# Optimization experiments

Hardware: AMD Instinct MI355X
Metric: run time of the kernel (lower is better)

## Reference

```python
import jax, jax.numpy as jnp
import numpy as np
from jax import lax

HEADS = 8
DIM_HEAD = 64
MODALITIES = 8
QUERY_DIM = 128
INNER = HEADS * DIM_HEAD  # 512


def _conv(x, w):
    # x: (b, Cin, H, W), w: (Cout, Cin, kh, kw), VALID padding (padding done manually)
    return lax.conv_general_dilated(x, w, window_strides=(1, 1), padding='VALID',
                                    dimension_numbers=('NCHW', 'OIHW', 'NCHW'))


def _reflect_pad_w(x):
    # ReflectionPad2d((2,2,0,0)): pad width (last) axis by 2 on each side
    return jnp.pad(x, ((0, 0), (0, 0), (0, 0), (2, 2)), mode='reflect')


def setup_inputs() -> dict:
    key = jax.random.key(0)
    k1, k2, k3, k4 = jax.random.split(key, 4)
    b, n, m, c = 2, 4096, MODALITIES, QUERY_DIM
    x = jax.random.normal(k1, (b, n, m, c), dtype=jnp.float32)
    Wq = jax.random.normal(k2, (INNER, c, 1, 5), dtype=jnp.float32) * 0.02
    Wkv = jax.random.normal(k3, (2 * INNER, c, 1, 5), dtype=jnp.float32) * 0.02
    Wout = jax.random.normal(k4, (c * m, INNER, m, 5), dtype=jnp.float32) * 0.02
    return {"x": x, "Wq": Wq, "Wkv": Wkv, "Wout": Wout}


def reference(x, Wq, Wkv, Wout):
    b, n, m, c = x.shape
    h, d = HEADS, DIM_HEAD
    scale = d ** -0.5

    xp = _reflect_pad_w(jnp.transpose(x, (0, 3, 2, 1)))  # (b, c, m, n+4)
    q = _conv(xp, Wq)                                     # (b, h*d, m, n)
    kv = _conv(xp, Wkv)                                   # (b, 2*h*d, m, n)
    k, v = kv[:, :h * d], kv[:, h * d:]

    # channel axis (h d) split: h outer, d inner -> (b, h, d, m, n)
    q = q.reshape(b, h, d, m, n)
    k = k.reshape(b, h, d, m, n)
    v = v.reshape(b, h, d, m, n)

    # attention over sequence axis n; feature dim is (m d) per head
    sim = jnp.einsum('bhdmi,bhdmj->bhij', q, k) * scale   # (b, h, n, n)
    attn = jax.nn.softmax(sim, axis=-1)
    out = jnp.einsum('bhij,bhdmj->bhdmi', attn, v)        # (b, h, d, m, n)

    out = out.reshape(b, h * d, m, n)                     # 'b (h d) m n'
    o = _conv(_reflect_pad_w(out), Wout)                  # (b, c*m, 1, n)
    o = o.reshape(b, c, m, 1, n)[:, :, :, 0, :]           # squeeze height-1 dim -> (b, c, m, n)
    return o.reshape(x.shape)                             # torch .view(x_shape) is a raw reshape
```

## Files before the change

kernel.cpp:

```cpp
#include <hip/hip_runtime.h>
#include <stdint.h>


typedef __attribute__((ext_vector_type(8))) short short8;
typedef __attribute__((ext_vector_type(4))) short short4v;
typedef __attribute__((ext_vector_type(2))) short short2v;
typedef __attribute__((ext_vector_type(4))) float f32x4;
typedef __attribute__((ext_vector_type(16))) float f32x16;

__device__ __forceinline__ f32x4 mfma16(short8 a, short8 b, f32x4 c) {
  return __builtin_amdgcn_mfma_f32_16x16x32_bf16(a, b, c, 0, 0, 0);
}
__device__ __forceinline__ f32x16 mfma32(short8 a, short8 b, f32x16 c) {
  return __builtin_amdgcn_mfma_f32_32x32x16_bf16(a, b, c, 0, 0, 0);
}

__device__ __forceinline__ unsigned short f2bf(float f) {
  union { float f; uint32_t u; } v; v.f = f;
  uint32_t r = (v.u + 0x7fffu + ((v.u >> 16) & 1u)) >> 16;
  return (unsigned short)r;
}

__device__ __forceinline__ uint32_t cvtpk(float lo, float hi) {
  uint32_t r;
  asm volatile("v_cvt_pk_bf16_f32 %0, %1, %2" : "=v"(r) : "v"(lo), "v"(hi));
  return r;
}
__device__ __forceinline__ void plswap(uint32_t& a, uint32_t& b) {
  asm volatile("v_permlane32_swap_b32 %0, %1" : "+v"(a), "+v"(b));
}

__device__ __forceinline__ int refl4096(int p) {
  p = p < 0 ? -p : p;
  return p >= 4096 ? 8190 - p : p;
}

__device__ __forceinline__ void gl_lds16(const void* g, void* l) {
  __builtin_amdgcn_global_load_lds(
      (const __attribute__((address_space(1))) void*)g,
      (__attribute__((address_space(3))) void*)l, 16, 0, 0);
}

__global__ void k_convw_qkv(const float* __restrict__ Wq,
                            const float* __restrict__ Wkv,
                            unsigned short* __restrict__ out) {
  int e = blockIdx.x * 256 + threadIdx.x;
  int oc = e / 640, k = e - oc * 640;
  int ci = k & 127, t = k >> 7;
  float w = (oc < 512) ? Wq[oc * 640 + ci * 5 + t]
                       : Wkv[(oc - 512) * 640 + ci * 5 + t];
  out[e] = f2bf(w);
}

__global__ __launch_bounds__(256)
void k_convx(const float* __restrict__ x, unsigned short* __restrict__ xb,
             int b) {
  int e = (blockIdx.x * 256 + threadIdx.x) * 8;
  const float* src = x + (size_t)b * 4194304 + e;
  f32x4 v0 = *(const f32x4*)src;
  f32x4 v1 = *(const f32x4*)(src + 4);
  short8 pk;
  pk[0] = (short)f2bf(v0[0]); pk[1] = (short)f2bf(v0[1]);
  pk[2] = (short)f2bf(v0[2]); pk[3] = (short)f2bf(v0[3]);
  pk[4] = (short)f2bf(v1[0]); pk[5] = (short)f2bf(v1[1]);
  pk[6] = (short)f2bf(v1[2]); pk[7] = (short)f2bf(v1[3]);
  *(short8*)(xb + e) = pk;
}

__global__ __launch_bounds__(256)
void k_convw_out(const float* __restrict__ Wout,
                 unsigned short* __restrict__ out) {
  __shared__ unsigned short row_l[20480];
  const int oc = blockIdx.x;
  const int tid = threadIdx.x;
  const float* src = Wout + (size_t)oc * 20480;
#pragma unroll
  for (int i0 = 0; i0 < 5120; i0 += 256) {
    int i = i0 + tid;
    f32x4 v = *(const f32x4*)(src + (size_t)i * 4);
    short4v pk;
    pk[0] = (short)f2bf(v[0]); pk[1] = (short)f2bf(v[1]);
    pk[2] = (short)f2bf(v[2]); pk[3] = (short)f2bf(v[3]);
    *(short4v*)(row_l + i * 4) = pk;
  }
  __syncthreads();
  unsigned short* drow = out + (size_t)oc * 20480;
#pragma unroll
  for (int r0 = 0; r0 < 20480; r0 += 512) {
    int e = r0 + tid * 2;
    int t0 = e >> 12, ft0 = e & 4095;
    int t1 = (e + 1) >> 12, ft1 = (e + 1) & 4095;
    short2v pk;
    pk[0] = (short)row_l[(ft0 >> 3) * 40 + (ft0 & 7) * 5 + t0];
    pk[1] = (short)row_l[(ft1 >> 3) * 40 + (ft1 & 7) * 5 + t1];
    *(short2v*)(drow + e) = pk;
  }
}

__global__ __launch_bounds__(256, 2)
void k_qkv(const unsigned short* __restrict__ xb,
           const unsigned short* __restrict__ Wb,
           unsigned short* __restrict__ Qg, unsigned short* __restrict__ Kg,
           unsigned short* __restrict__ Vg) {
  __shared__ __align__(16) unsigned short As[128 * 64];
  __shared__ __align__(16) unsigned short Bs[128 * 64];
  const int tid = threadIdx.x;
  const int lane = tid & 63, w = tid >> 6;
  const int wr = w >> 1, wc = w & 1;
  const int l15 = lane & 15, lg = lane >> 4;
  const int p0 = blockIdx.x * 128;
  const int ocb = blockIdx.y * 128;
  const int m = blockIdx.z;

  f32x4 acc[4][4];
#pragma unroll
  for (int i = 0; i < 4; i++)
#pragma unroll
    for (int j = 0; j < 4; j++) acc[i][j] = (f32x4){0.f, 0.f, 0.f, 0.f};

  for (int ks = 0; ks < 10; ks++) {
    const int t = ks >> 1;
    const int ci0 = (ks & 1) << 6;
    __syncthreads();
#pragma unroll
    for (int i = 0; i < 4; i++) {
      int s = tid + (i << 8);
      int row = s >> 3, c = s & 7;
      int cs = c ^ (row & 7);
      int xn = refl4096(p0 + row - 2 + t);
      gl_lds16(xb + (((size_t)xn << 3) + m) * 128 + ci0 + (cs << 3),
               (char*)As + (size_t)s * 16);
    }
#pragma unroll
    for (int c = 0; c < 4; c++) {
      int sb = ((c << 2) + w) << 6;
      int slot = sb + lane;
      int row = slot >> 3, cc = slot & 7;
      int cs = cc ^ (row & 7);
      gl_lds16(Wb + (size_t)(ocb + row) * 640 + (ks << 6) + (cs << 3),
               (char*)Bs + (size_t)sb * 16);
    }
    __syncthreads();
#pragma unroll
    for (int kk = 0; kk < 2; kk++) {
      short8 af[4], bq[4];
#pragma unroll
      for (int i = 0; i < 4; i++) {
        int row = (wr << 6) + (i << 4) + l15;
        af[i] = *(const short8*)((char*)As + (row << 7) +
                                 ((((kk << 2) + lg) ^ (row & 7)) << 4));
      }
#pragma unroll
      for (int j = 0; j < 4; j++) {
        int row = (wc << 6) + (j << 4) + l15;
        bq[j] = *(const short8*)((char*)Bs + (row << 7) +
                                 ((((kk << 2) + lg) ^ (row & 7)) << 4));
      }
#pragma unroll
      for (int i = 0; i < 4; i++)
#pragma unroll
        for (int j = 0; j < 4; j++) acc[i][j] = mfma16(af[i], bq[j], acc[i][j]);
    }
  }

  const int region = ocb >> 9;
  const float QSCALE = 0.18033688f;
#pragma unroll
  for (int i = 0; i < 4; i++) {
    const int posb = p0 + (wr << 6) + (i << 4) + (lg << 2);
#pragma unroll
    for (int j = 0; j < 4; j++) {
      const int oc = ocb + (wc << 6) + (j << 4) + l15;
      const int ocr = oc & 511;
      const int hh = ocr >> 6, dd = ocr & 63;
      const int f = (dd << 3) + m;
      if (region == 0) {
        size_t base = (size_t)hh * 4096 * 512 + f;
#pragma unroll
        for (int r = 0; r < 4; r++)
          Qg[base + (size_t)(posb + r) * 512] = f2bf(acc[i][j][r] * QSCALE);
      } else if (region == 1) {
        size_t base = (size_t)hh * 4096 * 512 + f;
#pragma unroll
        for (int r = 0; r < 4; r++)
          Kg[base + (size_t)(posb + r) * 512] = f2bf(acc[i][j][r]);
      } else {
        short4v pk;
#pragma unroll
        for (int r = 0; r < 4; r++) pk[r] = (short)f2bf(acc[i][j][r]);
        *(short4v*)(Vg + ((size_t)hh * 512 + f) * 4096 + posb) = pk;
      }
    }
  }
}

__global__ __launch_bounds__(512, 2)
void k_attn(const unsigned short* __restrict__ Qg,
            const unsigned short* __restrict__ Kg,
            const unsigned short* __restrict__ Vg,
            unsigned short* __restrict__ AO) {
  __shared__ __align__(16) char lds[131584];
  char* Kt = lds;
  char* Vt0 = lds + 32768;
  char* Vt1 = lds + 65536;
  char* Sx = lds + 98304;
  float* Ls = (float*)(lds + 131072);

  const int tid = threadIdx.x;
  const int lane = tid & 63, w = tid >> 6;
  const int l31 = lane & 31, hi = lane >> 5;
  const int wpair = w >> 1, whalf = w & 1;
  const int h = blockIdx.x & 7;
  const int qblk = blockIdx.x >> 3;
  const int qbase = qblk * 128 + wpair * 32;
  const int fh = whalf << 8;

  const size_t kb = (size_t)h * 4096 * 512;
  const size_t vb = (size_t)h * 512 * 4096;

  short8 q[16];
  {
    const unsigned short* qp =
        Qg + ((size_t)h * 4096 + qbase + l31) * 512 + fh + hi * 8;
#pragma unroll
    for (int ks = 0; ks < 16; ks++) q[ks] = *(const short8*)(qp + ks * 16);
  }

  f32x16 o[8];
#pragma unroll
  for (int t = 0; t < 8; t++)
#pragma unroll
    for (int e = 0; e < 16; e++) o[t][e] = 0.f;
  float lacc = 0.f;

  const int rb = l31 >> 1;
  const int swz = rb & 7;
  const int cg0 = ((l31 & 1) << 2) + hi;
  const int voff1 = rb * 128 + ((cg0 ^ swz) << 4);
  const int voff2 = rb * 128 + (((cg0 + 2) ^ swz) << 4);

  char* sxw = Sx + (w << 10) + (lane << 4);
  char* sxp = Sx + ((w ^ 1) << 10) + (lane << 4);

  union U { uint32_t d[4]; short8 s; };

  auto stageK = [&](int it) {
    const int key0 = it << 5;
#pragma unroll
    for (int i = 0; i < 4; i++) {
      int s = tid + (i << 9);
      int r = s >> 6, c = s & 63;
      gl_lds16(Kg + kb + (size_t)(key0 + r) * 512 + ((c ^ r) << 3),
               Kt + (size_t)s * 16);
    }
  };
  auto stageV = [&](int it, char* Vt) {
    const int key0 = it << 5;
#pragma unroll
    for (int i = 0; i < 4; i++) {
      int s = tid + (i << 9);
      int rp = s >> 3, c = s & 7;
      int cu = c ^ (rp & 7);
      int f = (rp << 1) + (cu >> 2);
      gl_lds16(Vg + vb + (size_t)f * 4096 + key0 + ((cu & 3) << 3),
               Vt + (size_t)s * 16);
    }
  };

  stageK(0);
  stageV(0, Vt0);

  for (int it = 0; it < 128; it++) {
    char* Vt = (it & 1) ? Vt1 : Vt0;
    char* Vn = (it & 1) ? Vt0 : Vt1;
    __syncthreads();

    if (it < 127) stageV(it + 1, Vn);

    f32x16 st;
#pragma unroll
    for (int e = 0; e < 16; e++) st[e] = 0.f;
#pragma unroll
    for (int ks = 0; ks < 16; ks++) {
      int ch = ((fh >> 3) + (ks << 1) + hi) ^ l31;
      short8 kfrag = *(const short8*)(Kt + (l31 << 10) + (ch << 4));
      st = mfma32(kfrag, q[ks], st);
    }
#pragma unroll
    for (int j = 0; j < 4; j++) {
      f32x4 pw = (f32x4){st[4 * j], st[4 * j + 1], st[4 * j + 2], st[4 * j + 3]};
      *(f32x4*)(sxw + (j << 13)) = pw;
    }
    __syncthreads();

    if (it < 127) stageK(it + 1);

#pragma unroll
    for (int j = 0; j < 4; j++) {
      f32x4 pv = *(const f32x4*)(sxp + (j << 13));
      st[4 * j] += pv[0]; st[4 * j + 1] += pv[1];
      st[4 * j + 2] += pv[2]; st[4 * j + 3] += pv[3];
    }

    float p[16];
#pragma unroll
    for (int r = 0; r < 16; r++) p[r] = __builtin_amdgcn_exp2f(st[r]);
    lacc += ((p[0] + p[1]) + (p[2] + p[3])) + ((p[4] + p[5]) + (p[6] + p[7])) +
            (((p[8] + p[9]) + (p[10] + p[11])) +
             ((p[12] + p[13]) + (p[14] + p[15])));

    uint32_t d0 = cvtpk(p[0], p[1]),  d1 = cvtpk(p[2], p[3]);
    uint32_t d2 = cvtpk(p[4], p[5]),  d3 = cvtpk(p[6], p[7]);
    uint32_t d4 = cvtpk(p[8], p[9]),  d5 = cvtpk(p[10], p[11]);
    uint32_t d6 = cvtpk(p[12], p[13]), d7 = cvtpk(p[14], p[15]);
    plswap(d0, d2); plswap(d1, d3);
    plswap(d4, d6); plswap(d5, d7);
    U u1; u1.d[0] = d0; u1.d[1] = d1; u1.d[2] = d2; u1.d[3] = d3;
    U u2; u2.d[0] = d4; u2.d[1] = d5; u2.d[2] = d6; u2.d[3] = d7;

#pragma unroll
    for (int tt = 0; tt < 8; tt++) {
      const char* vrow = Vt + (((whalf << 3) + tt) << 11);
      short8 v1 = *(const short8*)(vrow + voff1);
      short8 v2 = *(const short8*)(vrow + voff2);
      o[tt] = mfma32(u1.s, v1, o[tt]);
      o[tt] = mfma32(u2.s, v2, o[tt]);
    }
  }

  lacc += __shfl_xor(lacc, 32, 64);
  if (whalf == 0) Ls[(wpair << 5) + l31] = lacc;
  __syncthreads();

  float linv[16];
#pragma unroll
  for (int r = 0; r < 16; r++) {
    int qq = (r & 3) + ((r >> 2) << 3) + (hi << 2);
    linv[r] = 1.f / Ls[(wpair << 5) + qq];
  }
#pragma unroll
  for (int tt = 0; tt < 8; tt++) {
    size_t col = (size_t)h * 512 + (((whalf << 3) + tt) << 5) + l31;
#pragma unroll
    for (int r = 0; r < 16; r++) {
      int qq = qbase + (r & 3) + ((r >> 2) << 3) + (hi << 2);
      AO[(size_t)qq * 4096 + col] = f2bf(o[tt][r] * linv[r]);
    }
  }
}

__global__ __launch_bounds__(256, 2)
void k_outconv(const unsigned short* __restrict__ AO,
               const unsigned short* __restrict__ WB,
               float* __restrict__ outp, int b) {
  __shared__ __align__(16) unsigned short As[2][8192];
  __shared__ __align__(16) unsigned short Bs[2][4096];
  const int tid = threadIdx.x;
  const int lane = tid & 63, w = tid >> 6;
  const int wr = w >> 1, wc = w & 1;
  const int l15 = lane & 15, lg = lane >> 4;
  const int i0 = (blockIdx.x >> 4) * 128;
  const int ocb = (blockIdx.x & 15) * 64;

  f32x4 acc[4][2];
#pragma unroll
  for (int i = 0; i < 4; i++)
#pragma unroll
    for (int j = 0; j < 2; j++) acc[i][j] = (f32x4){0.f, 0.f, 0.f, 0.f};

  auto stage = [&](int ks, int d) {
    const int t = ks >> 6;
    const int f0 = (ks & 63) << 6;
    const int k0 = ks << 6;
#pragma unroll
    for (int i = 0; i < 4; i++) {
      int s = tid + (i << 8);
      int row = s >> 3, c = s & 7;
      int cs = c ^ (row & 7);
      int sr = refl4096(i0 + row + t - 2);
      gl_lds16(AO + (size_t)sr * 4096 + f0 + (cs << 3),
               (char*)As[d] + (size_t)s * 16);
    }
#pragma unroll
    for (int i = 0; i < 2; i++) {
      int s = tid + (i << 8);
      int row = s >> 3, c = s & 7;
      int cs = c ^ (row & 7);
      gl_lds16(WB + (size_t)(ocb + row) * 20480 + k0 + (cs << 3),
               (char*)Bs[d] + (size_t)s * 16);
    }
  };

  stage(0, 0);

  for (int ks = 0; ks < 320; ks++) {
    const int d = ks & 1;
    __syncthreads();
    if (ks < 319) stage(ks + 1, d ^ 1);
#pragma unroll
    for (int kk = 0; kk < 2; kk++) {
      short8 af[4], bq[2];
#pragma unroll
      for (int i = 0; i < 4; i++) {
        int row = (wr << 6) + (i << 4) + l15;
        af[i] = *(const short8*)((char*)As[d] + (row << 7) +
                                 ((((kk << 2) + lg) ^ (row & 7)) << 4));
      }
#pragma unroll
      for (int j = 0; j < 2; j++) {
        int row = (wc << 5) + (j << 4) + l15;
        bq[j] = *(const short8*)((char*)Bs[d] + (row << 7) +
                                 ((((kk << 2) + lg) ^ (row & 7)) << 4));
      }
#pragma unroll
      for (int i = 0; i < 4; i++)
#pragma unroll
        for (int j = 0; j < 2; j++) acc[i][j] = mfma16(af[i], bq[j], acc[i][j]);
    }
  }
#pragma unroll
  for (int i = 0; i < 4; i++)
#pragma unroll
    for (int j = 0; j < 2; j++) {
      int oc = ocb + (wc << 5) + (j << 4) + l15;
      int pos = i0 + (wr << 6) + (i << 4) + (lg << 2);
      *(f32x4*)(outp + ((size_t)b * 1024 + oc) * 4096 + pos) = acc[i][j];
    }
}

extern "C" void kernel_launch(void* const* d_in, const int* in_sizes, int n_in,
                              void* d_out, int out_size, void* d_ws,
                              size_t ws_size, hipStream_t stream) {
  const float* x = (const float*)d_in[0];
  const float* Wq = (const float*)d_in[1];
  const float* Wkv = (const float*)d_in[2];
  const float* Wout = (const float*)d_in[3];
  float* out = (float*)d_out;
  char* ws = (char*)d_ws;

  const size_t SEG = 33554432;
  unsigned short* Qg = (unsigned short*)ws;
  unsigned short* Kg = (unsigned short*)(ws + SEG);
  unsigned short* Vg = (unsigned short*)(ws + 2 * SEG);
  unsigned short* AO = (unsigned short*)(ws + 3 * SEG);
  unsigned short* xb = AO;
  unsigned short* WB1 = (unsigned short*)(ws + 4 * SEG);

  const size_t WB2_OFF = 136183808;
  const size_t WB2_BYTES = (size_t)1024 * 20480 * 2;
  const bool wb2_once = ws_size >= WB2_OFF + WB2_BYTES;
  unsigned short* WB2 =
      wb2_once ? (unsigned short*)(ws + WB2_OFF) : (unsigned short*)ws;

  k_convw_qkv<<<3840, 256, 0, stream>>>(Wq, Wkv, WB1);
  if (wb2_once) k_convw_out<<<1024, 256, 0, stream>>>(Wout, WB2);
  for (int b = 0; b < 2; b++) {
    k_convx<<<2048, 256, 0, stream>>>(x, xb, b);
    k_qkv<<<dim3(32, 12, 8), 256, 0, stream>>>(xb, WB1, Qg, Kg, Vg);
    k_attn<<<256, 512, 0, stream>>>(Qg, Kg, Vg, AO);
    if (!wb2_once) k_convw_out<<<1024, 256, 0, stream>>>(Wout, WB2);
    k_outconv<<<512, 256, 0, stream>>>(AO, WB2, out, b);
  }
}
```

Before: 1.603 ms.

## Split-K the output conv GEMM with larger 128x128 tiles plus reduce pass

The output convolution GEMM now uses 128x128 output tiles instead of 128x64. Its K range is split into two halves so the grid size stays the same. Each half writes fp32 partial sums into workspace, reusing the V buffer region, and a new elementwise kernel adds the two partials into the output. The goal is to halve the A-tile reloads per output element and raise MFMA work per LDS load. The cost is an extra kernel launch, the partial-sum write and read traffic, and more registers per thread.

```diff
diff --git a/kernel.cpp b/kernel.cpp
--- a/kernel.cpp
+++ b/kernel.cpp
@@ -95,6 +95,15 @@
     pk[1] = (short)row_l[(ft1 >> 3) * 40 + (ft1 & 7) * 5 + t1];
     *(short2v*)(drow + e) = pk;
   }
+}
+
+__global__ __launch_bounds__(256)
+void k_reduce(const float* __restrict__ P, float* __restrict__ outp, int b) {
+  int e = (blockIdx.x * 256 + threadIdx.x) * 4;
+  f32x4 a = *(const f32x4*)(P + e);
+  f32x4 c = *(const f32x4*)(P + 4194304 + e);
+  f32x4 s = (f32x4){a[0] + c[0], a[1] + c[1], a[2] + c[2], a[3] + c[3]};
+  *(f32x4*)(outp + (size_t)b * 4194304 + e) = s;
 }
 
 __global__ __launch_bounds__(256, 2)
@@ -352,26 +361,28 @@
 __global__ __launch_bounds__(256, 2)
 void k_outconv(const unsigned short* __restrict__ AO,
                const unsigned short* __restrict__ WB,
-               float* __restrict__ outp, int b) {
+               float* __restrict__ P) {
   __shared__ __align__(16) unsigned short As[2][8192];
-  __shared__ __align__(16) unsigned short Bs[2][4096];
+  __shared__ __align__(16) unsigned short Bs[2][8192];
   const int tid = threadIdx.x;
   const int lane = tid & 63, w = tid >> 6;
   const int wr = w >> 1, wc = w & 1;
   const int l15 = lane & 15, lg = lane >> 4;
+  const int ocb = (blockIdx.x & 7) * 128;
+  const int kslice = (blockIdx.x >> 3) & 1;
   const int i0 = (blockIdx.x >> 4) * 128;
-  const int ocb = (blockIdx.x & 15) * 64;
-
-  f32x4 acc[4][2];
+  const int ksbase = kslice * 160;
+
+  f32x4 acc[4][4];
 #pragma unroll
   for (int i = 0; i < 4; i++)
 #pragma unroll
-    for (int j = 0; j < 2; j++) acc[i][j] = (f32x4){0.f, 0.f, 0.f, 0.f};
-
-  auto stage = [&](int ks, int d) {
-    const int t = ks >> 6;
-    const int f0 = (ks & 63) << 6;
-    const int k0 = ks << 6;
+    for (int j = 0; j < 4; j++) acc[i][j] = (f32x4){0.f, 0.f, 0.f, 0.f};
+
+  auto stage = [&](int kabs, int d) {
+    const int t = kabs >> 6;
+    const int f0 = (kabs & 63) << 6;
+    const int k0 = kabs << 6;
 #pragma unroll
     for (int i = 0; i < 4; i++) {
       int s = tid + (i << 8);
@@ -382,7 +393,7 @@
                (char*)As[d] + (size_t)s * 16);
     }
 #pragma unroll
-    for (int i = 0; i < 2; i++) {
+    for (int i = 0; i < 4; i++) {
       int s = tid + (i << 8);
       int row = s >> 3, c = s & 7;
       int cs = c ^ (row & 7);
@@ -391,15 +402,15 @@
     }
   };
 
-  stage(0, 0);
-
-  for (int ks = 0; ks < 320; ks++) {
+  stage(ksbase, 0);
+
+  for (int ks = 0; ks < 160; ks++) {
     const int d = ks & 1;
     __syncthreads();
-    if (ks < 319) stage(ks + 1, d ^ 1);
+    if (ks < 159) stage(ksbase + ks + 1, d ^ 1);
 #pragma unroll
     for (int kk = 0; kk < 2; kk++) {
-      short8 af[4], bq[2];
+      short8 af[4], bq[4];
 #pragma unroll
       for (int i = 0; i < 4; i++) {
         int row = (wr << 6) + (i << 4) + l15;
@@ -407,24 +418,24 @@
                                  ((((kk << 2) + lg) ^ (row & 7)) << 4));
       }
 #pragma unroll
-      for (int j = 0; j < 2; j++) {
-        int row = (wc << 5) + (j << 4) + l15;
+      for (int j = 0; j < 4; j++) {
+        int row = (wc << 6) + (j << 4) + l15;
         bq[j] = *(const short8*)((char*)Bs[d] + (row << 7) +
                                  ((((kk << 2) + lg) ^ (row & 7)) << 4));
       }
 #pragma unroll
       for (int i = 0; i < 4; i++)
 #pragma unroll
-        for (int j = 0; j < 2; j++) acc[i][j] = mfma16(af[i], bq[j], acc[i][j]);
+        for (int j = 0; j < 4; j++) acc[i][j] = mfma16(af[i], bq[j], acc[i][j]);
     }
   }
 #pragma unroll
   for (int i = 0; i < 4; i++)
 #pragma unroll
-    for (int j = 0; j < 2; j++) {
-      int oc = ocb + (wc << 5) + (j << 4) + l15;
+    for (int j = 0; j < 4; j++) {
+      int oc = ocb + (wc << 6) + (j << 4) + l15;
       int pos = i0 + (wr << 6) + (i << 4) + (lg << 2);
-      *(f32x4*)(outp + ((size_t)b * 1024 + oc) * 4096 + pos) = acc[i][j];
+      *(f32x4*)(P + ((size_t)kslice * 1024 + oc) * 4096 + pos) = acc[i][j];
     }
 }
 
@@ -444,6 +455,7 @@
   unsigned short* Vg = (unsigned short*)(ws + 2 * SEG);
   unsigned short* AO = (unsigned short*)(ws + 3 * SEG);
   unsigned short* xb = AO;
+  float* Pp = (float*)(ws + 2 * SEG);
   unsigned short* WB1 = (unsigned short*)(ws + 4 * SEG);
 
   const size_t WB2_OFF = 136183808;
@@ -459,6 +471,7 @@
     k_qkv<<<dim3(32, 12, 8), 256, 0, stream>>>(xb, WB1, Qg, Kg, Vg);
     k_attn<<<256, 512, 0, stream>>>(Qg, Kg, Vg, AO);
     if (!wb2_once) k_convw_out<<<1024, 256, 0, stream>>>(Wout, WB2);
-    k_outconv<<<512, 256, 0, stream>>>(AO, WB2, out, b);
-  }
-}
+    k_outconv<<<512, 256, 0, stream>>>(AO, WB2, Pp);
+    k_reduce<<<4096, 256, 0, stream>>>(Pp, out, b);
+  }
+}
```

After: 1.415 ms. 11.7% less time.
